# Performance work log

Hardware: AMD Instinct MI355X
Metric: run time of the kernel (lower is better)

## Reference

```python
import jax, jax.numpy as jnp
import numpy as np

B, L, H, ED, NCONV = 64, 2048, 128, 4, 3
N = B * L


def gat(x, src, dst, edge_attr, W, a_s, a_d, We, a_e, b, self_loops):
    """PyG GATConv, heads=1, concat=True, negative_slope=0.2, fill_value='mean'."""
    n = x.shape[0]
    h = x @ W                              # [N,H]
    a_src = h @ a_s                        # [N]
    a_dst = h @ a_d                        # [N]
    alpha = a_src[src] + a_dst[dst] + (edge_attr @ We) @ a_e  # [E]
    if self_loops:
        ones = jnp.ones(src.shape[0], x.dtype)
        deg = jax.ops.segment_sum(ones, dst, num_segments=n)
        mean_attr = jax.ops.segment_sum(edge_attr, dst, num_segments=n) / jnp.maximum(deg, 1.0)[:, None]
        loop_alpha = a_src + a_dst + (mean_attr @ We) @ a_e
        idx = jnp.arange(n, dtype=src.dtype)
        src = jnp.concatenate([src, idx])
        dst = jnp.concatenate([dst, idx])
        alpha = jnp.concatenate([alpha, loop_alpha])
    alpha = jax.nn.leaky_relu(alpha, 0.2)
    m = jax.ops.segment_max(alpha, dst, num_segments=n)
    ex = jnp.exp(alpha - m[dst])
    den = jax.ops.segment_sum(ex, dst, num_segments=n)
    coef = ex / jnp.maximum(den, 1e-16)[dst]
    return jax.ops.segment_sum(coef[:, None] * h[src], dst, num_segments=n) + b


def setup_inputs() -> dict:
    key = jax.random.key(0)
    ks = iter(jax.random.split(key, 32))
    # binary trees: per graph, node k>0 has parent (k-1)//2; edge child->parent (to_up)
    local = np.arange(1, L)
    parent = (local - 1) // 2
    offs = (np.arange(B) * L)[:, None]
    src = jnp.asarray((local[None, :] + offs).ravel(), dtype=jnp.int32)
    dst = jnp.asarray((parent[None, :] + offs).ravel(), dtype=jnp.int32)
    E = src.shape[0]
    s = 0.1
    inp = {
        "x": jax.random.normal(next(ks), (N,), jnp.float32),
        "src": src,
        "dst": dst,
        "edge_attr": jax.random.normal(next(ks), (E, ED), jnp.float32),
        "up_W0": jax.random.normal(next(ks), (1, H)) * s,
        "up_W": jax.random.normal(next(ks), (NCONV - 1, H, H)) * s,
        "up_att_src": jax.random.normal(next(ks), (NCONV, H)) * s,
        "up_att_dst": jax.random.normal(next(ks), (NCONV, H)) * s,
        "up_We": jax.random.normal(next(ks), (NCONV, ED, H)) * s,
        "up_att_edge": jax.random.normal(next(ks), (NCONV, H)) * s,
        "up_b": jax.random.normal(next(ks), (NCONV, H)) * s,
        "down_W": jax.random.normal(next(ks), (NCONV - 1, H, H)) * s,
        "down_att_src": jax.random.normal(next(ks), (NCONV - 1, H)) * s,
        "down_att_dst": jax.random.normal(next(ks), (NCONV - 1, H)) * s,
        "down_We": jax.random.normal(next(ks), (NCONV - 1, ED, H)) * s,
        "down_att_edge": jax.random.normal(next(ks), (NCONV - 1, H)) * s,
        "down_b": jax.random.normal(next(ks), (NCONV - 1, H)) * s,
        "lin_W": jax.random.normal(next(ks), (NCONV - 1, H, H)) * s,
        "lin_b": jax.random.normal(next(ks), (NCONV - 1, H)) * s,
        "lin_last_W": jax.random.normal(next(ks), (H, 1)) * s,
        "lin_last_b": jax.random.normal(next(ks), (1,)) * s,
    }
    return inp


def reference(x, src, dst, edge_attr, up_W0, up_W, up_att_src, up_att_dst, up_We,
              up_att_edge, up_b, down_W, down_att_src, down_att_dst, down_We,
              down_att_edge, down_b, lin_W, lin_b, lin_last_W, lin_last_b):
    h = x[:, None]                                            # flat_c.view(-1,1)
    # upward pass: toup GATConvs (with self loops) + relu
    for i in range(NCONV):
        W = up_W0 if i == 0 else up_W[i - 1]
        h = jax.nn.relu(gat(h, src, dst, edge_attr, W, up_att_src[i], up_att_dst[i],
                            up_We[i], up_att_edge[i], up_b[i], True))
    x_up = h
    # downward pass uses reversed edges, no self loops; replicates original's
    # indexing bug (todown[0] used twice, todown[-1] never used)
    src_d, dst_d = dst, src
    x_down = jax.nn.relu(gat(x_up, src_d, dst_d, edge_attr, down_W[0], down_att_src[0],
                             down_att_dst[0], down_We[0], down_att_edge[0], down_b[0], False))
    xx = x_down + x_up
    for i in range(NCONV - 1):
        xx = jax.nn.relu(xx @ lin_W[i] + lin_b[i])
        x_down = jax.nn.relu(gat(xx, src_d, dst_d, edge_attr, down_W[i], down_att_src[i],
                                 down_att_dst[i], down_We[i], down_att_edge[i], down_b[i], False))
        xx = x_down + x_up
    final_emb = xx
    out_nodes = xx @ lin_last_W + lin_last_b                  # [N,1]
    batch_out = out_nodes.reshape(B, L)                       # all graphs are max_len
    batch_emb = final_emb.reshape(B, L, H)
    out = batch_out - batch_out[:, :1]                        # subtract root node
    return out, batch_emb
```

## Files before the change

### kernel.cpp

```cpp
#include <hip/hip_runtime.h>
#include <hip/hip_bf16.h>
#include <cstdint>
#include <cstddef>

typedef unsigned short u16;
typedef short bf16x8 __attribute__((ext_vector_type(8)));
typedef float f32x4 __attribute__((ext_vector_type(4)));

#define Bn 64
#define Ln 2048
#define Hn 128
#define EDn 4
#define Nn (Bn*Ln)

#define CV_W0    0
#define CV_WUP   128
#define CV_AS    32896
#define CV_AD    33280
#define CV_WE    33664
#define CV_AE    35200
#define CV_BUP   35584
#define CV_WD    35968
#define CV_BD    68736
#define CV_WL    68992
#define CV_BL    101760
#define CV_WLAST 102016
#define CV_TOTAL 102144

__device__ __forceinline__ float b2f(u16 u) {
  union { float f; unsigned int i; } v; v.i = ((unsigned int)u) << 16; return v.f;
}
__device__ __forceinline__ u16 f2b(float f) {
  __hip_bfloat16 h = __float2bfloat16(f);
  union { __hip_bfloat16 h; u16 u; } v; v.h = h; return v.u;
}
__device__ __forceinline__ float lrelu(float v) { return v >= 0.f ? v : 0.2f * v; }
__device__ __forceinline__ float wave_sum(float r) {
  #pragma unroll
  for (int off = 32; off > 0; off >>= 1) r += __shfl_xor(r, off, 64);
  return r;
}
__device__ __forceinline__ float ld_in(const void* p, size_t i, int f) {
  return f ? b2f(((const u16*)p)[i]) : ((const float*)p)[i];
}
__device__ __forceinline__ u16* Cbase(void* dout, int f) {
  return f ? ((u16*)dout + Nn) : (u16*)((float*)dout + Nn);
}
__device__ __forceinline__ float lo16(unsigned v) { return b2f((u16)(v & 0xFFFF)); }
__device__ __forceinline__ float hi16(unsigned v) { return b2f((u16)(v >> 16)); }

__device__ __forceinline__ void gload_lds16(const void* g, void* l) {
  __builtin_amdgcn_global_load_lds(
      (const __attribute__((address_space(1))) void*)g,
      (__attribute__((address_space(3))) void*)l, 16, 0, 0);
}

__device__ __forceinline__ int xcd_remap(int bid, int nwg) {
  return (bid & 7) * (nwg >> 3) + (bid >> 3);
}

__device__ __forceinline__ float2 coef_row(int p, const float2* __restrict__ asr,
                                           const void* __restrict__ edge_attr, int f,
                                           float w0, float w1, float w2, float w3) {
  int local = p & (Ln - 1);
  int root = p - local;
  int nb = p >> 11;
  int c1l = 2*local + 1, c2l = 2*local + 2;
  int deg = (c1l < Ln ? 1 : 0) + (c2l < Ln ? 1 : 0);
  float2 aa = asr[p];
  float e1 = 0.f, e2 = 0.f, sc1 = 0.f, sc2 = 0.f;
  if (deg >= 1) {
    size_t ei = ((size_t)nb*(Ln-1) + (c1l-1))*EDn;
    if (f) {
      ushort4 v = *(const ushort4*)((const u16*)edge_attr + ei);
      e1 = b2f(v.x)*w0 + b2f(v.y)*w1 + b2f(v.z)*w2 + b2f(v.w)*w3;
      if (deg == 2) {
        ushort4 v2 = *(const ushort4*)((const u16*)edge_attr + ei + EDn);
        e2 = b2f(v2.x)*w0 + b2f(v2.y)*w1 + b2f(v2.z)*w2 + b2f(v2.w)*w3;
      }
    } else {
      float4 v = *(const float4*)((const float*)edge_attr + ei);
      e1 = v.x*w0 + v.y*w1 + v.z*w2 + v.w*w3;
      if (deg == 2) {
        float4 v2 = *(const float4*)((const float*)edge_attr + ei + EDn);
        e2 = v2.x*w0 + v2.y*w1 + v2.z*w2 + v2.w*w3;
      }
    }
    sc1 = lrelu(asr[root + c1l].x + aa.y + e1);
    if (deg == 2) sc2 = lrelu(asr[root + c2l].x + aa.y + e2);
  }
  float mean_e = deg ? (e1 + e2) / (float)deg : 0.f;
  float ss = lrelu(aa.x + aa.y + mean_e);
  float m = ss;
  if (deg >= 1) m = fmaxf(m, sc1);
  if (deg == 2) m = fmaxf(m, sc2);
  float es  = __expf(ss - m);
  float ec1 = (deg >= 1) ? __expf(sc1 - m) : 0.f;
  float ec2 = (deg == 2) ? __expf(sc2 - m) : 0.f;
  float inv = 1.f / (es + ec1 + ec2);
  float2 cf; cf.x = ec1 * inv; cf.y = ec2 * inv;
  return cf;
}

__global__ void detect_kernel(const u16* __restrict__ x, int* __restrict__ flag) {
  int lane = threadIdx.x;
  u16 u = x[lane];
  int e = (u >> 7) & 0xFF;
  bool good = (e >= 100 && e <= 140) || ((u & 0x7FFF) == 0);
  unsigned long long m = __ballot(good);
  if (lane == 0) *flag = (__popcll(m) >= 56) ? 1 : 0;
}

struct CvtArgs { const void* src[12]; int off[12]; int tr[12]; };
__global__ void cvt_kernel(CvtArgs a, const int* __restrict__ flagp, u16* __restrict__ dst) {
  int f = *flagp;
  int i = blockIdx.x * 256 + threadIdx.x;
  if (i >= CV_TOTAL) return;
  int s = 0;
  #pragma unroll
  for (int k = 1; k < 12; ++k) s = (i >= a.off[k]) ? k : s;
  int j = i - a.off[s];
  int sj = j;
  if (a.tr[s]) {
    int mat = j >> 14, jm = j & 16383;
    int r = jm >> 7, c = jm & 127;
    int us = c >> 3, sub = c & 7;
    int u = us ^ (r & 15);
    int k = u * 8 + sub;
    sj = (mat << 14) + k * 128 + r;
  }
  dst[i] = f ? ((const u16*)a.src[s])[sj] : f2b(((const float*)a.src[s])[sj]);
}

__global__ void prep_kernel(const u16* __restrict__ cvt, float* __restrict__ P) {
  int lane = threadIdx.x & 63;
  #pragma unroll
  for (int d = 0; d < 14; ++d) {
    int ao, bo;
    if (d == 0)      { ao = CV_W0; bo = CV_AS; }
    else if (d == 1) { ao = CV_W0; bo = CV_AD; }
    else { int i = (d-2) >> 2, e = (d-2) & 3; ao = CV_WE + i*EDn*Hn + e*Hn; bo = CV_AE + i*Hn; }
    float r = b2f(cvt[ao+lane])*b2f(cvt[bo+lane])
            + b2f(cvt[ao+lane+64])*b2f(cvt[bo+lane+64]);
    r = wave_sum(r);
    if (lane == 0) P[d] = r;
  }
}

__global__ void up0_kernel(const void* __restrict__ x, const void* __restrict__ edge_attr,
                           const u16* __restrict__ W0, const u16* __restrict__ b0,
                           const float* __restrict__ Pd,
                           u16* __restrict__ y, const int* __restrict__ flagp) {
  __shared__ float comb[64];
  __shared__ float W0s[Hn];
  __shared__ float b0s[Hn];
  int f = *flagp;
  int t = threadIdx.x;
  if (t < Hn) { W0s[t] = b2f(W0[t]); b0s[t] = b2f(b0[t]); }
  int base = xcd_remap(blockIdx.x, gridDim.x) * 64;
  if (t < 64) {
    int n = base + t;
    int local = n & (Ln - 1);
    int nb = n >> 11;
    int root = n - local;
    float S0 = Pd[0], D0 = Pd[1];
    float w0 = Pd[2], w1 = Pd[3], w2 = Pd[4], w3 = Pd[5];
    float xp = ld_in(x, n, f);
    float ad_p = D0 * xp;
    int c1l = 2*local + 1, c2l = 2*local + 2;
    int deg = (c1l < Ln ? 1 : 0) + (c2l < Ln ? 1 : 0);
    float e1 = 0.f, e2 = 0.f, xc1 = 0.f, xc2 = 0.f, sc1 = 0.f, sc2 = 0.f;
    if (deg >= 1) {
      xc1 = ld_in(x, root + c1l, f);
      size_t ei = ((size_t)nb*(Ln-1) + (c1l-1))*EDn;
      e1 = ld_in(edge_attr, ei+0, f)*w0 + ld_in(edge_attr, ei+1, f)*w1
         + ld_in(edge_attr, ei+2, f)*w2 + ld_in(edge_attr, ei+3, f)*w3;
      sc1 = lrelu(S0*xc1 + ad_p + e1);
    }
    if (deg == 2) {
      xc2 = ld_in(x, root + c2l, f);
      size_t ei = ((size_t)nb*(Ln-1) + (c2l-1))*EDn;
      e2 = ld_in(edge_attr, ei+0, f)*w0 + ld_in(edge_attr, ei+1, f)*w1
         + ld_in(edge_attr, ei+2, f)*w2 + ld_in(edge_attr, ei+3, f)*w3;
      sc2 = lrelu(S0*xc2 + ad_p + e2);
    }
    float mean_e = deg ? (e1 + e2) / (float)deg : 0.f;
    float ss = lrelu(S0*xp + ad_p + mean_e);
    float m = ss;
    if (deg >= 1) m = fmaxf(m, sc1);
    if (deg == 2) m = fmaxf(m, sc2);
    float es  = __expf(ss - m);
    float ec1 = (deg >= 1) ? __expf(sc1 - m) : 0.f;
    float ec2 = (deg == 2) ? __expf(sc2 - m) : 0.f;
    float den = es + ec1 + ec2;
    comb[t] = (es*xp + ec1*xc1 + ec2*xc2) / den;
  }
  __syncthreads();
  u16* out = y + (size_t)base * Hn;
  for (int i = t; i < 64*Hn/4; i += 256) {
    int row = i >> 5;
    int col = (i & 31) * 4;
    float c = comb[row];
    ushort4 st;
    st.x = f2b(fmaxf(c*W0s[col+0] + b0s[col+0], 0.f));
    st.y = f2b(fmaxf(c*W0s[col+1] + b0s[col+1], 0.f));
    st.z = f2b(fmaxf(c*W0s[col+2] + b0s[col+2], 0.f));
    st.w = f2b(fmaxf(c*W0s[col+3] + b0s[col+3], 0.f));
    *(ushort4*)&out[(size_t)i*4] = st;
  }
}

__device__ __forceinline__ void load_x(uint4 (&xf)[2][4], const u16* __restrict__ X,
                                       int wbase, int m, int q) {
  #pragma unroll
  for (int rt = 0; rt < 2; ++rt) {
    int R = wbase + rt*16 + m;
    const uint4* src = (const uint4*)(X + (size_t)R*Hn);
    #pragma unroll
    for (int ki = 0; ki < 4; ++ki) xf[rt][ki] = src[ki*4 + q];
  }
}

__device__ __forceinline__ void read_pw(uint4 (&xf)[2][4], const u16* PW,
                                        int wbase, int p0l, int m, int q) {
  #pragma unroll
  for (int rt = 0; rt < 2; ++rt) {
    int R = wbase + rt*16 + m;
    int l = R & (Ln - 1);
    bool zero = (l == 0);
    int pr = zero ? 0 : (((l - 1) >> 1) - p0l);
    #pragma unroll
    for (int ki = 0; ki < 4; ++ki) {
      int u = ki*4 + q;
      uint4 v = *(const uint4*)&PW[((size_t)pr*16 + (u ^ (pr & 15)))*8];
      if (zero) { v.x = 0; v.y = 0; v.z = 0; v.w = 0; }
      xf[rt][ki] = v;
    }
  }
}

template<int EPI, int ASAD>
__device__ __forceinline__ void compute_tile(
    const uint4 (&xf)[2][4], const u16* Ws, int wbase, int m, int q, int f,
    const u16* __restrict__ bias, const u16* __restrict__ Uarr,
    u16* __restrict__ od, float* __restrict__ emf, int out_mode,
    float2* __restrict__ asad, const u16* __restrict__ avs,
    const u16* __restrict__ avd, float* __restrict__ nodesp) {
  ushort4 uvr[2][8];
  if (EPI == 2) {
    #pragma unroll
    for (int rt = 0; rt < 2; ++rt) {
      int R = wbase + rt*16 + m;
      #pragma unroll
      for (int ct = 0; ct < 8; ++ct)
        uvr[rt][ct] = *(const ushort4*)&Uarr[(size_t)R*Hn + ct*16 + q*4];
    }
  }
  float asv[2] = {0.f, 0.f}, adv[2] = {0.f, 0.f};
  #pragma unroll
  for (int cb = 0; cb < 2; ++cb) {
    f32x4 acc[2][4];
    #pragma unroll
    for (int rt = 0; rt < 2; ++rt)
      #pragma unroll
      for (int c4 = 0; c4 < 4; ++c4) acc[rt][c4] = (f32x4){0.f, 0.f, 0.f, 0.f};
    #pragma unroll
    for (int ki = 0; ki < 4; ++ki) {
      #pragma unroll
      for (int c4 = 0; c4 < 4; ++c4) {
        int ct = cb*4 + c4;
        bf16x8 wf = *(bf16x8*)&Ws[((ct*16 + m)*16 + ((ki*4 + q) ^ m))*8];
        #pragma unroll
        for (int rt = 0; rt < 2; ++rt)
          acc[rt][c4] = __builtin_amdgcn_mfma_f32_16x16x32_bf16(
                          wf, *(bf16x8*)&xf[rt][ki], acc[rt][c4], 0, 0, 0);
      }
    }
    #pragma unroll
    for (int rt = 0; rt < 2; ++rt) {
      int R = wbase + rt*16 + m;
      #pragma unroll
      for (int c4 = 0; c4 < 4; ++c4) {
        int ct = cb*4 + c4;
        int c0 = ct*16 + q*4;
        float o[4];
        #pragma unroll
        for (int r = 0; r < 4; ++r) o[r] = acc[rt][c4][r];
        if (ASAD == 1) {
          ushort4 sv = *(const ushort4*)&avs[c0];
          ushort4 dv = *(const ushort4*)&avd[c0];
          asv[rt] += o[0]*b2f(sv.x) + o[1]*b2f(sv.y) + o[2]*b2f(sv.z) + o[3]*b2f(sv.w);
          adv[rt] += o[0]*b2f(dv.x) + o[1]*b2f(dv.y) + o[2]*b2f(dv.z) + o[3]*b2f(dv.w);
        }
        if (EPI >= 1) {
          ushort4 bv = *(const ushort4*)&bias[c0];
          o[0] = fmaxf(o[0] + b2f(bv.x), 0.f); o[1] = fmaxf(o[1] + b2f(bv.y), 0.f);
          o[2] = fmaxf(o[2] + b2f(bv.z), 0.f); o[3] = fmaxf(o[3] + b2f(bv.w), 0.f);
        }
        if (EPI == 2) {
          ushort4 uv = uvr[rt][ct];
          o[0] += b2f(uv.x); o[1] += b2f(uv.y); o[2] += b2f(uv.z); o[3] += b2f(uv.w);
        }
        if (ASAD == 2) {
          ushort4 sv = *(const ushort4*)&avs[c0];
          asv[rt] += o[0]*b2f(sv.x) + o[1]*b2f(sv.y) + o[2]*b2f(sv.z) + o[3]*b2f(sv.w);
        }
        if (out_mode == 2 && !f) {
          float4 fv; fv.x = o[0]; fv.y = o[1]; fv.z = o[2]; fv.w = o[3];
          *(float4*)&emf[(size_t)R*Hn + c0] = fv;
        } else {
          ushort4 st; st.x = f2b(o[0]); st.y = f2b(o[1]); st.z = f2b(o[2]); st.w = f2b(o[3]);
          *(ushort4*)&od[(size_t)R*Hn + c0] = st;
        }
      }
    }
  }
  #pragma unroll
  for (int rt = 0; rt < 2; ++rt) {
    int R = wbase + rt*16 + m;
    if (ASAD == 1) {
      float as_ = asv[rt], ad_ = adv[rt];
      as_ += __shfl_xor(as_, 16, 64); as_ += __shfl_xor(as_, 32, 64);
      ad_ += __shfl_xor(ad_, 16, 64); ad_ += __shfl_xor(ad_, 32, 64);
      if (q == 0) { float2 v; v.x = as_; v.y = ad_; asad[R] = v; }
    }
    if (ASAD == 2) {
      float as_ = asv[rt];
      as_ += __shfl_xor(as_, 16, 64); as_ += __shfl_xor(as_, 32, 64);
      if (q == 0) nodesp[R] = as_;
    }
  }
}

template<int GATHER, int EPI, int ASAD>
__global__ __launch_bounds__(256, 2) void gemm_k(
                       const u16* __restrict__ Xp, const u16* __restrict__ Wt,
                       const u16* __restrict__ bias, const u16* __restrict__ Uarr,
                       u16* __restrict__ outp, void* __restrict__ dout,
                       const int* __restrict__ flagp, int x_is_C, int out_mode,
                       float2* __restrict__ asad, const u16* __restrict__ avs,
                       const u16* __restrict__ avd, float* __restrict__ nodesp) {
  __shared__ u16 Ws[Hn*Hn + (GATHER ? 130*Hn : 0)];
  u16* PW = Ws + Hn*Hn;
  int f = *flagp;
  const u16* X = x_is_C ? Cbase(dout, f) : Xp;
  int t = threadIdx.x;
  int lane = t & 63, w = t >> 6;
  int m = lane & 15, q = lane >> 4;
  int row0 = xcd_remap(blockIdx.x, gridDim.x) * 256;
  int wb0 = row0 + w*32;
  int wb1 = row0 + 128 + w*32;
  #pragma unroll
  for (int i = 0; i < 8; ++i)
    gload_lds16(Wt + (size_t)(i*256 + t)*8, &Ws[(size_t)(i*256 + (t & ~63))*8]);
  uint4 xf0[2][4], xf1[2][4];
  int p0l = 0;
  if (GATHER) {
    int l0 = row0 & (Ln - 1);
    p0l = l0 ? ((l0 >> 1) - 1) : 0;
    size_t pbase = (size_t)((row0 - l0) + p0l) * Hn;
    for (int i = 0; i < 9; ++i) {
      int s = i*256 + t;
      if (s < 129*16) {
        int r = s >> 4, v = s & 15;
        gload_lds16(X + pbase + (size_t)r*Hn + (size_t)((v ^ (r & 15))*8),
                    &PW[(size_t)(i*256 + (t & ~63))*8]);
      }
    }
  } else {
    load_x(xf0, X, wb0, m, q);
  }
  __syncthreads();
  if (GATHER) {
    read_pw(xf0, PW, wb0, p0l, m, q);
    read_pw(xf1, PW, wb1, p0l, m, q);
  } else {
    load_x(xf1, X, wb1, m, q);
  }
  u16* Cb = Cbase(dout, f);
  float* emf = (float*)dout + Nn;
  u16* od = (out_mode == 0) ? outp : (out_mode == 1 ? Cb : (u16*)dout + Nn);
  compute_tile<EPI, ASAD>(xf0, Ws, wb0, m, q, f, bias, Uarr, od, emf, out_mode,
                          asad, avs, avd, nodesp);
  compute_tile<EPI, ASAD>(xf1, Ws, wb1, m, q, f, bias, Uarr, od, emf, out_mode,
                          asad, avs, avd, nodesp);
}

__global__ __launch_bounds__(256, 2) void gemm_blend_k(
                       const u16* __restrict__ Wt, const void* __restrict__ edge_attr,
                       const float2* __restrict__ asad_in, const float* __restrict__ Pd,
                       const u16* __restrict__ bias_up, u16* __restrict__ outp,
                       void* __restrict__ dout, const int* __restrict__ flagp,
                       float2* __restrict__ asad2, const u16* __restrict__ avs,
                       const u16* __restrict__ avd) {
  __shared__ u16 Ws[Hn*Hn];
  __shared__ u16 CW[Hn*Hn];
  int f = *flagp;
  const u16* h = Cbase(dout, f);
  int t = threadIdx.x;
  int lane = t & 63, w = t >> 6;
  int m = lane & 15, q = lane >> 4;
  int row0 = xcd_remap(blockIdx.x, gridDim.x) * 64;
  int l0 = row0 & (Ln - 1);
  int root = row0 - l0;
  int j = w*16 + m;
  int R = row0 + j;
  int l = l0 + j;
  int deg = (2*l+1 < Ln ? 1 : 0) + (2*l+2 < Ln ? 1 : 0);
  #pragma unroll
  for (int i = 0; i < 8; ++i)
    gload_lds16(Wt + (size_t)(i*256 + t)*8, &Ws[(size_t)(i*256 + (t & ~63))*8]);
  if (l0 < Ln/2) {
    size_t cbase = (size_t)(root + 2*l0 + 1) * Hn;
    size_t emax = (size_t)Nn*Hn - 8;
    #pragma unroll
    for (int i = 0; i < 8; ++i) {
      int s = i*256 + t;
      int r = s >> 4, v = s & 15;
      size_t elem = cbase + (size_t)r*Hn + (size_t)((v ^ (r & 15))*8);
      if (elem > emax) elem = emax;
      gload_lds16(h + elem, &CW[(size_t)(i*256 + (t & ~63))*8]);
    }
  }
  uint4 own[4], bv4[4];
  #pragma unroll
  for (int ki = 0; ki < 4; ++ki) {
    own[ki] = *(const uint4*)&h[(size_t)R*Hn + (size_t)((ki*4 + q)*8)];
    bv4[ki] = ((const uint4*)bias_up)[ki*4 + q];
  }
  float2 cf = coef_row(R, asad_in, edge_attr, f, Pd[6], Pd[7], Pd[8], Pd[9]);
  float es = 1.f - cf.x - cf.y;
  __syncthreads();
  int r1 = 2*j, r2 = 2*j + 1;
  uint4 xf[4];
  #pragma unroll
  for (int ki = 0; ki < 4; ++ki) {
    int u = ki*4 + q;
    uint4 b = {0,0,0,0}, c = {0,0,0,0};
    if (deg >= 1) b = *(const uint4*)&CW[((size_t)r1*16 + (u ^ (r1 & 15)))*8];
    if (deg == 2) c = *(const uint4*)&CW[((size_t)r2*16 + (u ^ (r2 & 15)))*8];
    uint4 a = own[ki], bb = bv4[ki];
    uint4 st;
    #pragma unroll
    for (int i = 0; i < 4; ++i) {
      unsigned av = ((unsigned*)&a)[i], b1v = ((unsigned*)&b)[i];
      unsigned b2v = ((unsigned*)&c)[i], bbv = ((unsigned*)&bb)[i];
      float o0 = es*lo16(av) + cf.x*lo16(b1v) + cf.y*lo16(b2v) + lo16(bbv);
      float o1 = es*hi16(av) + cf.x*hi16(b1v) + cf.y*hi16(b2v) + hi16(bbv);
      ((unsigned*)&st)[i] = (unsigned)f2b(fmaxf(o0, 0.f))
                          | ((unsigned)f2b(fmaxf(o1, 0.f)) << 16);
    }
    xf[ki] = st;
  }
  f32x4 acc[8];
  #pragma unroll
  for (int ct = 0; ct < 8; ++ct) acc[ct] = (f32x4){0.f, 0.f, 0.f, 0.f};
  #pragma unroll
  for (int ki = 0; ki < 4; ++ki) {
    #pragma unroll
    for (int ct = 0; ct < 8; ++ct) {
      bf16x8 wf = *(bf16x8*)&Ws[((ct*16 + m)*16 + ((ki*4 + q) ^ m))*8];
      acc[ct] = __builtin_amdgcn_mfma_f32_16x16x32_bf16(
                    wf, *(bf16x8*)&xf[ki], acc[ct], 0, 0, 0);
    }
  }
  float asv = 0.f, adv = 0.f;
  #pragma unroll
  for (int ct = 0; ct < 8; ++ct) {
    int c0 = ct*16 + q*4;
    float o0 = acc[ct][0], o1 = acc[ct][1], o2 = acc[ct][2], o3 = acc[ct][3];
    ushort4 sv = *(const ushort4*)&avs[c0];
    ushort4 dv = *(const ushort4*)&avd[c0];
    asv += o0*b2f(sv.x) + o1*b2f(sv.y) + o2*b2f(sv.z) + o3*b2f(sv.w);
    adv += o0*b2f(dv.x) + o1*b2f(dv.y) + o2*b2f(dv.z) + o3*b2f(dv.w);
    ushort4 st; st.x = f2b(o0); st.y = f2b(o1); st.z = f2b(o2); st.w = f2b(o3);
    *(ushort4*)&outp[(size_t)R*Hn + c0] = st;
  }
  asv += __shfl_xor(asv, 16, 64); asv += __shfl_xor(asv, 32, 64);
  adv += __shfl_xor(adv, 16, 64); adv += __shfl_xor(adv, 32, 64);
  if (q == 0) { float2 v; v.x = asv; v.y = adv; asad2[R] = v; }
}

__global__ __launch_bounds__(512, 4) void fused_down_lin_k(
                       const u16* __restrict__ Xp, const u16* __restrict__ Wdt,
                       const u16* __restrict__ bd, const u16* __restrict__ Uarr,
                       const u16* __restrict__ Wlt, const u16* __restrict__ bl,
                       u16* __restrict__ outp) {
  __shared__ u16 Ws[Hn*Hn];
  __shared__ u16 XX[Hn*Hn];
  u16* PW = XX;
  int t = threadIdx.x;
  int lane = t & 63, w = t >> 6;
  int m = lane & 15, q = lane >> 4;
  int row0 = xcd_remap(blockIdx.x, gridDim.x) * 128;
  int l0 = row0 & (Ln - 1);
  int root = row0 - l0;
  int p0l = l0 ? ((l0 >> 1) - 1) : 0;
  int R = row0 + w*16 + m;
  int rl = w*16 + m;
  #pragma unroll
  for (int i = 0; i < 4; ++i)
    gload_lds16(Wdt + (size_t)(i*512 + t)*8, &Ws[(size_t)(i*512 + (t & ~63))*8]);
  {
    size_t pbase = (size_t)(root + p0l) * Hn;
    for (int i = 0; i < 3; ++i) {
      int s = i*512 + t;
      if (s < 65*16) {
        int r = s >> 4, v = s & 15;
        gload_lds16(Xp + pbase + (size_t)r*Hn + (size_t)((v ^ (r & 15))*8),
                    &PW[(size_t)(i*512 + (t & ~63))*8]);
      }
    }
  }
  ushort4 uvr[8];
  #pragma unroll
  for (int ct = 0; ct < 8; ++ct)
    uvr[ct] = *(const ushort4*)&Uarr[(size_t)R*Hn + ct*16 + q*4];
  __syncthreads();
  int l = R & (Ln - 1);
  bool zero = (l == 0);
  int pr = zero ? 0 : (((l - 1) >> 1) - p0l);
  uint4 xf[4];
  #pragma unroll
  for (int ki = 0; ki < 4; ++ki) {
    int u = ki*4 + q;
    uint4 v = *(const uint4*)&PW[((size_t)pr*16 + (u ^ (pr & 15)))*8];
    if (zero) { v.x = 0; v.y = 0; v.z = 0; v.w = 0; }
    xf[ki] = v;
  }
  f32x4 acc[8];
  #pragma unroll
  for (int ct = 0; ct < 8; ++ct) acc[ct] = (f32x4){0.f, 0.f, 0.f, 0.f};
  #pragma unroll
  for (int ki = 0; ki < 4; ++ki) {
    #pragma unroll
    for (int ct = 0; ct < 8; ++ct) {
      bf16x8 wf = *(bf16x8*)&Ws[((ct*16 + m)*16 + ((ki*4 + q) ^ m))*8];
      acc[ct] = __builtin_amdgcn_mfma_f32_16x16x32_bf16(
                    wf, *(bf16x8*)&xf[ki], acc[ct], 0, 0, 0);
    }
  }
  __syncthreads();
  #pragma unroll
  for (int i = 0; i < 4; ++i)
    gload_lds16(Wlt + (size_t)(i*512 + t)*8, &Ws[(size_t)(i*512 + (t & ~63))*8]);
  #pragma unroll
  for (int ct = 0; ct < 8; ++ct) {
    int c0 = ct*16 + q*4;
    ushort4 bv = *(const ushort4*)&bd[c0];
    ushort4 uv = uvr[ct];
    float o0 = fmaxf(acc[ct][0] + b2f(bv.x), 0.f) + b2f(uv.x);
    float o1 = fmaxf(acc[ct][1] + b2f(bv.y), 0.f) + b2f(uv.y);
    float o2 = fmaxf(acc[ct][2] + b2f(bv.z), 0.f) + b2f(uv.z);
    float o3 = fmaxf(acc[ct][3] + b2f(bv.w), 0.f) + b2f(uv.w);
    int uu = (2*ct + (q >> 1)) ^ m;
    uint2 pk;
    pk.x = (unsigned)f2b(o0) | ((unsigned)f2b(o1) << 16);
    pk.y = (unsigned)f2b(o2) | ((unsigned)f2b(o3) << 16);
    *(uint2*)&XX[rl*Hn + uu*8 + (q & 1)*4] = pk;
  }
  __syncthreads();
  f32x4 acc2[8];
  #pragma unroll
  for (int ct = 0; ct < 8; ++ct) acc2[ct] = (f32x4){0.f, 0.f, 0.f, 0.f};
  #pragma unroll
  for (int ki = 0; ki < 4; ++ki) {
    #pragma unroll
    for (int ct = 0; ct < 8; ++ct) {
      bf16x8 wf = *(bf16x8*)&Ws[((ct*16 + m)*16 + ((ki*4 + q) ^ m))*8];
      bf16x8 xb = *(bf16x8*)&XX[rl*Hn + (((ki*4 + q) ^ m))*8];
      acc2[ct] = __builtin_amdgcn_mfma_f32_16x16x32_bf16(wf, xb, acc2[ct], 0, 0, 0);
    }
  }
  #pragma unroll
  for (int ct = 0; ct < 8; ++ct) {
    int c0 = ct*16 + q*4;
    ushort4 bv = *(const ushort4*)&bl[c0];
    ushort4 st;
    st.x = f2b(fmaxf(acc2[ct][0] + b2f(bv.x), 0.f));
    st.y = f2b(fmaxf(acc2[ct][1] + b2f(bv.y), 0.f));
    st.z = f2b(fmaxf(acc2[ct][2] + b2f(bv.z), 0.f));
    st.w = f2b(fmaxf(acc2[ct][3] + b2f(bv.w), 0.f));
    *(ushort4*)&outp[(size_t)R*Hn + c0] = st;
  }
}

__global__ void blend_kernel(const u16* __restrict__ h, const void* __restrict__ edge_attr,
                             const float2* __restrict__ asad2, const float* __restrict__ Pd,
                             const u16* __restrict__ bias, u16* __restrict__ y,
                             const int* __restrict__ flagp) {
  int f = *flagp;
  int t = threadIdx.x;
  int g = t & 15;
  int p = xcd_remap(blockIdx.x, gridDim.x) * 16 + (t >> 4);
  int local = p & (Ln - 1);
  int root = p - local;
  int c1l = 2*local + 1, c2l = 2*local + 2;
  int deg = (c1l < Ln ? 1 : 0) + (c2l < Ln ? 1 : 0);
  float2 cf = coef_row(p, asad2, edge_attr, f, Pd[10], Pd[11], Pd[12], Pd[13]);
  float es = 1.f - cf.x - cf.y;
  int off = g * 8;
  uint4 hp = *(const uint4*)&h[(size_t)p*Hn + off];
  uint4 h1 = {0,0,0,0}, h2 = {0,0,0,0};
  if (deg >= 1) h1 = *(const uint4*)&h[(size_t)(root + c1l)*Hn + off];
  if (deg == 2) h2 = *(const uint4*)&h[(size_t)(root + c2l)*Hn + off];
  uint4 bv = *(const uint4*)&bias[off];
  uint4 st;
  #pragma unroll
  for (int i = 0; i < 4; ++i) {
    unsigned a = ((unsigned*)&hp)[i], b1 = ((unsigned*)&h1)[i];
    unsigned b2 = ((unsigned*)&h2)[i], bb = ((unsigned*)&bv)[i];
    float o0 = es*lo16(a) + cf.x*lo16(b1) + cf.y*lo16(b2) + lo16(bb);
    float o1 = es*hi16(a) + cf.x*hi16(b1) + cf.y*hi16(b2) + hi16(bb);
    ((unsigned*)&st)[i] = (unsigned)f2b(fmaxf(o0, 0.f)) | ((unsigned)f2b(fmaxf(o1, 0.f)) << 16);
  }
  *(uint4*)&y[(size_t)p*Hn + off] = st;
}

__global__ void score_kernel(const float* __restrict__ nodes, void* __restrict__ dout,
                             const int* __restrict__ flagp) {
  int f = *flagp;
  int n = xcd_remap(blockIdx.x, gridDim.x) * 256 + threadIdx.x;
  float v = nodes[n] - nodes[n & ~(Ln - 1)];
  if (f) ((u16*)dout)[n] = f2b(v);
  else   ((float*)dout)[n] = v;
}

extern "C" void kernel_launch(void* const* d_in, const int* in_sizes, int n_in,
                              void* d_out, int out_size, void* d_ws, size_t ws_size,
                              hipStream_t stream) {
  const void* x         = d_in[0];
  const void* edge_attr = d_in[3];

  u16* Ubuf = (u16*)d_ws;
  u16* Abuf = Ubuf + (size_t)Nn*Hn;
  u16* Bbuf = Abuf + (size_t)Nn*Hn;
  u16* cvt  = Bbuf + (size_t)Nn*Hn;
  float2* asad  = (float2*)(cvt + CV_TOTAL);
  float2* asad2 = asad + Nn;
  float* nodes = (float*)(asad2 + Nn);
  int* flag = (int*)(nodes + Nn);
  float* Pdots = (float*)(flag + 4);

  detect_kernel<<<1, 64, 0, stream>>>((const u16*)d_in[0], flag);

  CvtArgs ca;
  ca.src[0]  = d_in[4];  ca.off[0]  = CV_W0;    ca.tr[0]  = 0;
  ca.src[1]  = d_in[5];  ca.off[1]  = CV_WUP;   ca.tr[1]  = 1;
  ca.src[2]  = d_in[6];  ca.off[2]  = CV_AS;    ca.tr[2]  = 0;
  ca.src[3]  = d_in[7];  ca.off[3]  = CV_AD;    ca.tr[3]  = 0;
  ca.src[4]  = d_in[8];  ca.off[4]  = CV_WE;    ca.tr[4]  = 0;
  ca.src[5]  = d_in[9];  ca.off[5]  = CV_AE;    ca.tr[5]  = 0;
  ca.src[6]  = d_in[10]; ca.off[6]  = CV_BUP;   ca.tr[6]  = 0;
  ca.src[7]  = d_in[11]; ca.off[7]  = CV_WD;    ca.tr[7]  = 1;
  ca.src[8]  = d_in[16]; ca.off[8]  = CV_BD;    ca.tr[8]  = 0;
  ca.src[9]  = d_in[17]; ca.off[9]  = CV_WL;    ca.tr[9]  = 1;
  ca.src[10] = d_in[18]; ca.off[10] = CV_BL;    ca.tr[10] = 0;
  ca.src[11] = d_in[19]; ca.off[11] = CV_WLAST; ca.tr[11] = 0;
  cvt_kernel<<<(CV_TOTAL + 255)/256, 256, 0, stream>>>(ca, flag, cvt);
  prep_kernel<<<1, 64, 0, stream>>>(cvt, Pdots);

  up0_kernel<<<Nn/64, 256, 0, stream>>>(x, edge_attr, cvt+CV_W0, cvt+CV_BUP,
                                        Pdots, Abuf, flag);
  gemm_k<0,0,1><<<Nn/256, 256, 0, stream>>>(Abuf, cvt+CV_WUP, nullptr, nullptr,
                                         nullptr, d_out, flag, 0, 1,
                                         asad, cvt+CV_AS+Hn, cvt+CV_AD+Hn, nullptr);
  gemm_blend_k<<<Nn/64, 256, 0, stream>>>(cvt+CV_WUP+Hn*Hn, edge_attr, asad, Pdots,
                                           cvt+CV_BUP+Hn, Bbuf, d_out, flag,
                                           asad2, cvt+CV_AS+2*Hn, cvt+CV_AD+2*Hn);
  blend_kernel<<<Nn/16, 256, 0, stream>>>(Bbuf, edge_attr, asad2, Pdots,
                                          cvt+CV_BUP+2*Hn, Ubuf, flag);

  fused_down_lin_k<<<Nn/128, 512, 0, stream>>>(Ubuf, cvt+CV_WD, cvt+CV_BD, Ubuf,
                                               cvt+CV_WL, cvt+CV_BL, Abuf);
  fused_down_lin_k<<<Nn/128, 512, 0, stream>>>(Abuf, cvt+CV_WD, cvt+CV_BD, Ubuf,
                                               cvt+CV_WL+Hn*Hn, cvt+CV_BL+Hn, Bbuf);
  gemm_k<1,2,2><<<Nn/256, 256, 0, stream>>>(Bbuf, cvt+CV_WD+Hn*Hn, cvt+CV_BD+Hn, Ubuf,
                                         nullptr, d_out, flag, 0, 2,
                                         nullptr, cvt+CV_WLAST, nullptr, nodes);

  score_kernel<<<Nn/256, 256, 0, stream>>>(nodes, d_out, flag);
}
```

Measured before the change: 279.5 us.

## Replace first up-layer GEMM with piecewise-linear lookup table over scalar input

The first GAT layer's output is relu(c*W0+b0) for a scalar c per node, so the following 128x128 GEMM is a piecewise-linear function of c with breakpoints at -b0/w0. A single-block kernel sorts the breakpoints and precomputes per-segment slope and intercept vectors. Each node then does a binary search and a 128-wide FMA instead of writing a full activation row and running a GEMM on it. The tables are stored in bf16, which may shift rounding relative to the original GEMM path, and the table kernel runs serially in one block.

```diff
diff --git a/kernel.cpp b/kernel.cpp
--- a/kernel.cpp
+++ b/kernel.cpp
@@ -147,67 +147,138 @@
   }
 }
 
-__global__ void up0_kernel(const void* __restrict__ x, const void* __restrict__ edge_attr,
-                           const u16* __restrict__ W0, const u16* __restrict__ b0,
-                           const float* __restrict__ Pd,
-                           u16* __restrict__ y, const int* __restrict__ flagp) {
-  __shared__ float comb[64];
-  __shared__ float W0s[Hn];
-  __shared__ float b0s[Hn];
+__global__ void table_kernel(const u16* __restrict__ cvt, float* __restrict__ tsort,
+                             u16* __restrict__ segA, u16* __restrict__ segB) {
+  __shared__ float tsh[128];
+  __shared__ int ord[128];
+  int k = threadIdx.x;
+  float w0k = b2f(cvt[CV_W0 + k]);
+  float b0k = b2f(cvt[CV_BUP + k]);
+  float tk = (w0k != 0.f) ? (-b0k / w0k) : __builtin_inff();
+  tsh[k] = tk;
+  __syncthreads();
+  int rank = 0;
+  for (int j = 0; j < 128; ++j) {
+    float tj = tsh[j];
+    if (tj < tk || (tj == tk && j < k)) rank++;
+  }
+  ord[rank] = k;
+  tsort[rank] = tk;
+  __syncthreads();
+  float runA = 0.f, runB = 0.f;
+  for (int j = 0; j < 128; ++j) {
+    float w = b2f(cvt[CV_W0 + j]);
+    float b = b2f(cvt[CV_BUP + j]);
+    if (w < 0.f || (w == 0.f && b > 0.f)) {
+      float w1v = b2f(cvt[CV_WUP + k*128 + (((j >> 3) ^ (k & 15)) * 8) + (j & 7)]);
+      runA += w * w1v; runB += b * w1v;
+    }
+  }
+  for (int s = 0; s <= 128; ++s) {
+    segA[s*128 + k] = f2b(runA);
+    segB[s*128 + k] = f2b(runB);
+    if (s < 128) {
+      int j = ord[s];
+      float w = b2f(cvt[CV_W0 + j]);
+      float b = b2f(cvt[CV_BUP + j]);
+      if (w != 0.f) {
+        float w1v = b2f(cvt[CV_WUP + k*128 + (((j >> 3) ^ (k & 15)) * 8) + (j & 7)]);
+        float sgn = (w > 0.f) ? 1.f : -1.f;
+        runA += sgn * w * w1v; runB += sgn * b * w1v;
+      }
+    }
+  }
+}
+
+__global__ void comb_kernel(const void* __restrict__ x, const void* __restrict__ edge_attr,
+                            const float* __restrict__ Pd, float* __restrict__ comb,
+                            const int* __restrict__ flagp) {
   int f = *flagp;
+  int n = xcd_remap(blockIdx.x, gridDim.x) * 256 + threadIdx.x;
+  int local = n & (Ln - 1);
+  int nb = n >> 11;
+  int root = n - local;
+  float S0 = Pd[0], D0 = Pd[1];
+  float w0 = Pd[2], w1 = Pd[3], w2 = Pd[4], w3 = Pd[5];
+  float xp = ld_in(x, n, f);
+  float ad_p = D0 * xp;
+  int c1l = 2*local + 1, c2l = 2*local + 2;
+  int deg = (c1l < Ln ? 1 : 0) + (c2l < Ln ? 1 : 0);
+  float e1 = 0.f, e2 = 0.f, xc1 = 0.f, xc2 = 0.f, sc1 = 0.f, sc2 = 0.f;
+  if (deg >= 1) {
+    xc1 = ld_in(x, root + c1l, f);
+    size_t ei = ((size_t)nb*(Ln-1) + (c1l-1))*EDn;
+    e1 = ld_in(edge_attr, ei+0, f)*w0 + ld_in(edge_attr, ei+1, f)*w1
+       + ld_in(edge_attr, ei+2, f)*w2 + ld_in(edge_attr, ei+3, f)*w3;
+    sc1 = lrelu(S0*xc1 + ad_p + e1);
+  }
+  if (deg == 2) {
+    xc2 = ld_in(x, root + c2l, f);
+    size_t ei = ((size_t)nb*(Ln-1) + (c2l-1))*EDn;
+    e2 = ld_in(edge_attr, ei+0, f)*w0 + ld_in(edge_attr, ei+1, f)*w1
+       + ld_in(edge_attr, ei+2, f)*w2 + ld_in(edge_attr, ei+3, f)*w3;
+    sc2 = lrelu(S0*xc2 + ad_p + e2);
+  }
+  float mean_e = deg ? (e1 + e2) / (float)deg : 0.f;
+  float ss = lrelu(S0*xp + ad_p + mean_e);
+  float m = ss;
+  if (deg >= 1) m = fmaxf(m, sc1);
+  if (deg == 2) m = fmaxf(m, sc2);
+  float es  = __expf(ss - m);
+  float ec1 = (deg >= 1) ? __expf(sc1 - m) : 0.f;
+  float ec2 = (deg == 2) ? __expf(sc2 - m) : 0.f;
+  float den = es + ec1 + ec2;
+  comb[n] = (es*xp + ec1*xc1 + ec2*xc2) / den;
+}
+
+__global__ void cfill_kernel(const float* __restrict__ comb, const float* __restrict__ tsort,
+                             const u16* __restrict__ segA, const u16* __restrict__ segB,
+                             const u16* __restrict__ avs, const u16* __restrict__ avd,
+                             void* __restrict__ dout, const int* __restrict__ flagp,
+                             float2* __restrict__ asad) {
+  __shared__ float ts[128];
   int t = threadIdx.x;
-  if (t < Hn) { W0s[t] = b2f(W0[t]); b0s[t] = b2f(b0[t]); }
-  int base = xcd_remap(blockIdx.x, gridDim.x) * 64;
-  if (t < 64) {
-    int n = base + t;
-    int local = n & (Ln - 1);
-    int nb = n >> 11;
-    int root = n - local;
-    float S0 = Pd[0], D0 = Pd[1];
-    float w0 = Pd[2], w1 = Pd[3], w2 = Pd[4], w3 = Pd[5];
-    float xp = ld_in(x, n, f);
-    float ad_p = D0 * xp;
-    int c1l = 2*local + 1, c2l = 2*local + 2;
-    int deg = (c1l < Ln ? 1 : 0) + (c2l < Ln ? 1 : 0);
-    float e1 = 0.f, e2 = 0.f, xc1 = 0.f, xc2 = 0.f, sc1 = 0.f, sc2 = 0.f;
-    if (deg >= 1) {
-      xc1 = ld_in(x, root + c1l, f);
-      size_t ei = ((size_t)nb*(Ln-1) + (c1l-1))*EDn;
-      e1 = ld_in(edge_attr, ei+0, f)*w0 + ld_in(edge_attr, ei+1, f)*w1
-         + ld_in(edge_attr, ei+2, f)*w2 + ld_in(edge_attr, ei+3, f)*w3;
-      sc1 = lrelu(S0*xc1 + ad_p + e1);
-    }
-    if (deg == 2) {
-      xc2 = ld_in(x, root + c2l, f);
-      size_t ei = ((size_t)nb*(Ln-1) + (c2l-1))*EDn;
-      e2 = ld_in(edge_attr, ei+0, f)*w0 + ld_in(edge_attr, ei+1, f)*w1
-         + ld_in(edge_attr, ei+2, f)*w2 + ld_in(edge_attr, ei+3, f)*w3;
-      sc2 = lrelu(S0*xc2 + ad_p + e2);
-    }
-    float mean_e = deg ? (e1 + e2) / (float)deg : 0.f;
-    float ss = lrelu(S0*xp + ad_p + mean_e);
-    float m = ss;
-    if (deg >= 1) m = fmaxf(m, sc1);
-    if (deg == 2) m = fmaxf(m, sc2);
-    float es  = __expf(ss - m);
-    float ec1 = (deg >= 1) ? __expf(sc1 - m) : 0.f;
-    float ec2 = (deg == 2) ? __expf(sc2 - m) : 0.f;
-    float den = es + ec1 + ec2;
-    comb[t] = (es*xp + ec1*xc1 + ec2*xc2) / den;
-  }
+  if (t < 128) ts[t] = tsort[t];
   __syncthreads();
-  u16* out = y + (size_t)base * Hn;
-  for (int i = t; i < 64*Hn/4; i += 256) {
-    int row = i >> 5;
-    int col = (i & 31) * 4;
-    float c = comb[row];
-    ushort4 st;
-    st.x = f2b(fmaxf(c*W0s[col+0] + b0s[col+0], 0.f));
-    st.y = f2b(fmaxf(c*W0s[col+1] + b0s[col+1], 0.f));
-    st.z = f2b(fmaxf(c*W0s[col+2] + b0s[col+2], 0.f));
-    st.w = f2b(fmaxf(c*W0s[col+3] + b0s[col+3], 0.f));
-    *(ushort4*)&out[(size_t)i*4] = st;
-  }
+  int f = *flagp;
+  u16* C = Cbase(dout, f);
+  int g = t & 15;
+  int p = xcd_remap(blockIdx.x, gridDim.x) * 16 + (t >> 4);
+  float c = comb[p];
+  int lo = 0, hi = 128;
+  #pragma unroll
+  for (int it = 0; it < 7; ++it) {
+    int mid = (lo + hi) >> 1;
+    if (ts[mid] < c) lo = mid + 1; else hi = mid;
+  }
+  int seg = lo;
+  int off = g * 8;
+  const u16* Ar = segA + seg*128 + off;
+  const u16* Br = segB + seg*128 + off;
+  ushort4 a0 = *(const ushort4*)Ar,     a1 = *(const ushort4*)(Ar + 4);
+  ushort4 bb0 = *(const ushort4*)Br,    bb1 = *(const ushort4*)(Br + 4);
+  ushort4 s0 = *(const ushort4*)&avs[off], s1 = *(const ushort4*)&avs[off + 4];
+  ushort4 d0 = *(const ushort4*)&avd[off], d1 = *(const ushort4*)&avd[off + 4];
+  float h[8];
+  h[0] = c*b2f(a0.x) + b2f(bb0.x); h[1] = c*b2f(a0.y) + b2f(bb0.y);
+  h[2] = c*b2f(a0.z) + b2f(bb0.z); h[3] = c*b2f(a0.w) + b2f(bb0.w);
+  h[4] = c*b2f(a1.x) + b2f(bb1.x); h[5] = c*b2f(a1.y) + b2f(bb1.y);
+  h[6] = c*b2f(a1.z) + b2f(bb1.z); h[7] = c*b2f(a1.w) + b2f(bb1.w);
+  float as_ = h[0]*b2f(s0.x) + h[1]*b2f(s0.y) + h[2]*b2f(s0.z) + h[3]*b2f(s0.w)
+            + h[4]*b2f(s1.x) + h[5]*b2f(s1.y) + h[6]*b2f(s1.z) + h[7]*b2f(s1.w);
+  float ad_ = h[0]*b2f(d0.x) + h[1]*b2f(d0.y) + h[2]*b2f(d0.z) + h[3]*b2f(d0.w)
+            + h[4]*b2f(d1.x) + h[5]*b2f(d1.y) + h[6]*b2f(d1.z) + h[7]*b2f(d1.w);
+  uint4 st;
+  ((unsigned*)&st)[0] = (unsigned)f2b(h[0]) | ((unsigned)f2b(h[1]) << 16);
+  ((unsigned*)&st)[1] = (unsigned)f2b(h[2]) | ((unsigned)f2b(h[3]) << 16);
+  ((unsigned*)&st)[2] = (unsigned)f2b(h[4]) | ((unsigned)f2b(h[5]) << 16);
+  ((unsigned*)&st)[3] = (unsigned)f2b(h[6]) | ((unsigned)f2b(h[7]) << 16);
+  *(uint4*)&C[(size_t)p*Hn + off] = st;
+  as_ += __shfl_xor(as_, 1, 64); as_ += __shfl_xor(as_, 2, 64);
+  as_ += __shfl_xor(as_, 4, 64); as_ += __shfl_xor(as_, 8, 64);
+  ad_ += __shfl_xor(ad_, 1, 64); ad_ += __shfl_xor(ad_, 2, 64);
+  ad_ += __shfl_xor(ad_, 4, 64); ad_ += __shfl_xor(ad_, 8, 64);
+  if (g == 0) { float2 v; v.x = as_; v.y = ad_; asad[p] = v; }
 }
 
 __device__ __forceinline__ void load_x(uint4 (&xf)[2][4], const u16* __restrict__ X,
@@ -641,6 +712,9 @@
   float* nodes = (float*)(asad2 + Nn);
   int* flag = (int*)(nodes + Nn);
   float* Pdots = (float*)(flag + 4);
+  float* tsort = Pdots + 16;
+  u16* segA = (u16*)(tsort + 128);
+  u16* segB = segA + 129*128;
 
   detect_kernel<<<1, 64, 0, stream>>>((const u16*)d_in[0], flag);
 
@@ -659,12 +733,12 @@
   ca.src[11] = d_in[19]; ca.off[11] = CV_WLAST; ca.tr[11] = 0;
   cvt_kernel<<<(CV_TOTAL + 255)/256, 256, 0, stream>>>(ca, flag, cvt);
   prep_kernel<<<1, 64, 0, stream>>>(cvt, Pdots);
-
-  up0_kernel<<<Nn/64, 256, 0, stream>>>(x, edge_attr, cvt+CV_W0, cvt+CV_BUP,
-                                        Pdots, Abuf, flag);
-  gemm_k<0,0,1><<<Nn/256, 256, 0, stream>>>(Abuf, cvt+CV_WUP, nullptr, nullptr,
-                                         nullptr, d_out, flag, 0, 1,
-                                         asad, cvt+CV_AS+Hn, cvt+CV_AD+Hn, nullptr);
+  table_kernel<<<1, 128, 0, stream>>>(cvt, tsort, segA, segB);
+
+  comb_kernel<<<Nn/256, 256, 0, stream>>>(x, edge_attr, Pdots, nodes, flag);
+  cfill_kernel<<<Nn/16, 256, 0, stream>>>(nodes, tsort, segA, segB,
+                                          cvt+CV_AS+Hn, cvt+CV_AD+Hn,
+                                          d_out, flag, asad);
   gemm_blend_k<<<Nn/64, 256, 0, stream>>>(cvt+CV_WUP+Hn*Hn, edge_attr, asad, Pdots,
                                            cvt+CV_BUP+Hn, Bbuf, d_out, flag,
                                            asad2, cvt+CV_AS+2*Hn, cvt+CV_AD+2*Hn);
```

Measured after the change: 317.0 us. 1.13x slower.
